# Kernel optimization log

Hardware: AMD Instinct MI355X
Metric: run time of the kernel (lower is better)

The kernel has to match this reference:

```python
import jax, jax.numpy as jnp
import numpy as np

N = 65536   # batch_size * timeseries
D = 512     # feature dim of h_real
K = 64      # n_clusters


def setup_inputs() -> dict:
    key = jax.random.key(0)
    k1, k2 = jax.random.split(key)
    h_real = jax.random.normal(k1, (N, D), dtype=jnp.float32)
    # F is an (approximately) orthogonal projection parameter [N, K].
    F = jax.random.normal(k2, (N, K), dtype=jnp.float32)
    return {"h_real": h_real, "F": F}


def reference(h_real, F):
    # Original: WTW = h h^T (N x N); loss = trace(WTW) - trace(F^T WTW F).
    # Algebraically identical reduced form, never materializing the N x N Gram:
    #   trace(h h^T) = sum(h * h)
    #   trace(F^T h h^T F) = ||F^T h||_F^2
    tr_wtw = jnp.sum(h_real * h_real)
    G = F.T @ h_real                      # [K, D] skinny GEMM
    tr_proj = jnp.sum(G * G)
    return tr_wtw - tr_proj
```

## Files before the change

kernel.cpp:

```cpp
#include <hip/hip_runtime.h>
#include <hip/hip_fp16.h>

#define N_TOT 65536
#define D_DIM 512
#define K_DIM 64
#define NC    32
#define HT_S  40
#define GSZ   (K_DIM * D_DIM)

typedef __bf16   bf16x8 __attribute__((ext_vector_type(8)));
typedef float    f32x4  __attribute__((ext_vector_type(4)));
typedef _Float16 half8  __attribute__((ext_vector_type(8)));

__device__ __forceinline__ unsigned int pack_bf16(float a, float b) {
    union { float f; unsigned int u; } x, y;
    x.f = a; y.f = b;
    unsigned int lo = (x.u + 0x7fffu + ((x.u >> 16) & 1u)) >> 16;
    unsigned int hi = (y.u + 0x7fffu + ((y.u >> 16) & 1u)) >> 16;
    return lo | (hi << 16);
}

extern "C" __global__ void __launch_bounds__(1024)
k1_partial(const float* __restrict__ h, const float* __restrict__ F,
           float* __restrict__ trw_out, unsigned short* __restrict__ gpart,
           float* __restrict__ out, int rowsPerBlock) {
    __shared__ unsigned short ht[2][D_DIM * HT_S];
    __shared__ unsigned short Ft[2][K_DIM * HT_S];
    __shared__ float red[16];

    const int tid = threadIdx.x;
    const int b   = blockIdx.x;
    if (b == 0 && tid == 0) out[0] = 0.0f;

    const int row0    = b * rowsPerBlock;
    const int nChunks = rowsPerBlock / NC;

    const int sd = tid & 511;
    const int sg = tid >> 9;
    const int fk = tid & 63;
    const int fg = (tid >> 6) & 3;
    const int wave = tid >> 6;
    const int lane = tid & 63;
    const int m    = lane & 15;
    const int q    = lane >> 4;

    f32x4 acc[4][2];
    #pragma unroll
    for (int kt = 0; kt < 4; ++kt)
        #pragma unroll
        for (int dt = 0; dt < 2; ++dt)
            acc[kt][dt] = (f32x4){0.f, 0.f, 0.f, 0.f};

    float trw = 0.f;

    auto stage = [&](int c, int p) {
        const int r0 = row0 + c * NC;
        const float* hb = h + (size_t)r0 * D_DIM + sd;
        #pragma unroll
        for (int gi = 0; gi < 2; ++gi) {
            const int g8 = gi * 2 + sg;
            float v[8];
            #pragma unroll
            for (int j = 0; j < 8; ++j) {
                v[j] = hb[(size_t)(g8 * 8 + j) * D_DIM];
                trw += v[j] * v[j];
            }
            uint4 pk;
            pk.x = pack_bf16(v[0], v[1]);
            pk.y = pack_bf16(v[2], v[3]);
            pk.z = pack_bf16(v[4], v[5]);
            pk.w = pack_bf16(v[6], v[7]);
            *(uint4*)&ht[p][sd * HT_S + g8 * 8] = pk;
        }
        if (tid < 256) {
            const float* fb = F + (size_t)r0 * K_DIM + fk;
            float w[8];
            #pragma unroll
            for (int j = 0; j < 8; ++j)
                w[j] = fb[(size_t)(fg * 8 + j) * K_DIM];
            uint4 pk;
            pk.x = pack_bf16(w[0], w[1]);
            pk.y = pack_bf16(w[2], w[3]);
            pk.z = pack_bf16(w[4], w[5]);
            pk.w = pack_bf16(w[6], w[7]);
            *(uint4*)&Ft[p][fk * HT_S + fg * 8] = pk;
        }
    };

    stage(0, 0);

    for (int c = 0; c < nChunks; ++c) {
        __syncthreads();
        if (c + 1 < nChunks) stage(c + 1, (c + 1) & 1);

        const int p = c & 1;
        bf16x8 bfrag[2], afrag[4];
        #pragma unroll
        for (int dt = 0; dt < 2; ++dt)
            bfrag[dt] = *(const bf16x8*)&ht[p][(wave * 32 + dt * 16 + m) * HT_S + q * 8];
        #pragma unroll
        for (int kt = 0; kt < 4; ++kt)
            afrag[kt] = *(const bf16x8*)&Ft[p][(kt * 16 + m) * HT_S + q * 8];
        #pragma unroll
        for (int kt = 0; kt < 4; ++kt)
            #pragma unroll
            for (int dt = 0; dt < 2; ++dt)
                acc[kt][dt] = __builtin_amdgcn_mfma_f32_16x16x32_bf16(
                    afrag[kt], bfrag[dt], acc[kt][dt], 0, 0, 0);
    }

    unsigned short* gp = gpart + (size_t)b * GSZ;
    #pragma unroll
    for (int kt = 0; kt < 4; ++kt)
        #pragma unroll
        for (int dt = 0; dt < 2; ++dt)
            #pragma unroll
            for (int r = 0; r < 4; ++r) {
                const int k = kt * 16 + q * 4 + r;
                const int d = wave * 32 + dt * 16 + m;
                __half hv = __float2half(acc[kt][dt][r]);
                gp[k * D_DIM + d] = *(unsigned short*)&hv;
            }

    #pragma unroll
    for (int off = 32; off > 0; off >>= 1) trw += __shfl_down(trw, off, 64);
    if (lane == 0) red[wave] = trw;
    __syncthreads();
    if (tid == 0) {
        float s = 0.f;
        #pragma unroll
        for (int w = 0; w < 16; ++w) s += red[w];
        trw_out[b] = s;
    }
}

extern "C" __global__ void __launch_bounds__(512)
k2_reduce(const float* __restrict__ trw, const unsigned short* __restrict__ gpart,
          float* __restrict__ out, int P) {
    __shared__ float sh[32 * 16 * 8];
    __shared__ float red2[8];

    const int tid = threadIdx.x;
    const int sub = tid >> 4;
    const int oct = tid & 15;
    const int tt  = blockIdx.x * 16 + oct;

    float g[8];
    #pragma unroll
    for (int j = 0; j < 8; ++j) g[j] = 0.f;

    const unsigned short* base = gpart + (size_t)tt * 8;
    for (int b = sub; b < P; b += 32) {
        half8 v = *(const half8*)(base + (size_t)b * GSZ);
        #pragma unroll
        for (int j = 0; j < 8; ++j) g[j] += (float)v[j];
    }
    #pragma unroll
    for (int j = 0; j < 8; ++j) sh[(sub * 16 + oct) * 8 + j] = g[j];
    __syncthreads();

    float val = 0.f;
    if (tid < 128) {
        const int o2 = tid >> 3, j = tid & 7;
        float s = 0.f;
        #pragma unroll
        for (int sb = 0; sb < 32; ++sb) s += sh[(sb * 16 + o2) * 8 + j];
        val = -s * s;
    } else if (blockIdx.x == 0 && tid - 128 < P) {
        val = trw[tid - 128];
    }

    #pragma unroll
    for (int off = 32; off > 0; off >>= 1) val += __shfl_down(val, off, 64);
    if ((tid & 63) == 0) red2[tid >> 6] = val;
    __syncthreads();
    if (tid == 0) {
        float s = 0.f;
        #pragma unroll
        for (int w = 0; w < 8; ++w) s += red2[w];
        atomicAdd(out, s);
    }
}

extern "C" void kernel_launch(void* const* d_in, const int* in_sizes, int n_in,
                              void* d_out, int out_size, void* d_ws, size_t ws_size,
                              hipStream_t stream) {
    const float* h = (const float*)d_in[0];
    const float* F = (const float*)d_in[1];
    float* out = (float*)d_out;

    int P = 256;
    while (P > 1 && (size_t)4096 + (size_t)P * (GSZ * 2) > ws_size) P >>= 1;
    const int rowsPerBlock = N_TOT / P;

    float* trw = (float*)d_ws;
    unsigned short* gpart = (unsigned short*)((char*)d_ws + 4096);

    hipLaunchKernelGGL(k1_partial, dim3(P), dim3(1024), 0, stream,
                       h, F, trw, gpart, out, rowsPerBlock);
    hipLaunchKernelGGL(k2_reduce, dim3(256), dim3(512), 0, stream,
                       trw, gpart, out, P);
}
```

Measured before the change: 210.9 us.

## Load MFMA fragments directly from global memory, dropping LDS staging

```diff
diff --git a/kernel.cpp b/kernel.cpp
--- a/kernel.cpp
+++ b/kernel.cpp
@@ -5,7 +5,6 @@
 #define D_DIM 512
 #define K_DIM 64
 #define NC    32
-#define HT_S  40
 #define GSZ   (K_DIM * D_DIM)
 
 typedef __bf16   bf16x8 __attribute__((ext_vector_type(8)));
@@ -20,29 +19,25 @@
     return lo | (hi << 16);
 }
 
+union pk4 { unsigned int u[4]; bf16x8 v; };
+
 extern "C" __global__ void __launch_bounds__(1024)
 k1_partial(const float* __restrict__ h, const float* __restrict__ F,
            float* __restrict__ trw_out, unsigned short* __restrict__ gpart,
            float* __restrict__ out, int rowsPerBlock) {
-    __shared__ unsigned short ht[2][D_DIM * HT_S];
-    __shared__ unsigned short Ft[2][K_DIM * HT_S];
     __shared__ float red[16];
 
     const int tid = threadIdx.x;
     const int b   = blockIdx.x;
     if (b == 0 && tid == 0) out[0] = 0.0f;
 
-    const int row0    = b * rowsPerBlock;
-    const int nChunks = rowsPerBlock / NC;
-
-    const int sd = tid & 511;
-    const int sg = tid >> 9;
-    const int fk = tid & 63;
-    const int fg = (tid >> 6) & 3;
     const int wave = tid >> 6;
     const int lane = tid & 63;
     const int m    = lane & 15;
     const int q    = lane >> 4;
+
+    const int row0    = b * rowsPerBlock;
+    const int nChunks = rowsPerBlock / NC;
 
     f32x4 acc[4][2];
     #pragma unroll
@@ -53,60 +48,58 @@
 
     float trw = 0.f;
 
-    auto stage = [&](int c, int p) {
-        const int r0 = row0 + c * NC;
-        const float* hb = h + (size_t)r0 * D_DIM + sd;
+    const float* hb = h + (size_t)(row0 + q * 8) * D_DIM + wave * 32 + m;
+    const float* fb = F + (size_t)(row0 + q * 8) * K_DIM + m;
+
+    for (int c = 0; c < nChunks; ++c) {
+        float vb[16];
         #pragma unroll
-        for (int gi = 0; gi < 2; ++gi) {
-            const int g8 = gi * 2 + sg;
-            float v[8];
-            #pragma unroll
-            for (int j = 0; j < 8; ++j) {
-                v[j] = hb[(size_t)(g8 * 8 + j) * D_DIM];
-                trw += v[j] * v[j];
-            }
-            uint4 pk;
-            pk.x = pack_bf16(v[0], v[1]);
-            pk.y = pack_bf16(v[2], v[3]);
-            pk.z = pack_bf16(v[4], v[5]);
-            pk.w = pack_bf16(v[6], v[7]);
-            *(uint4*)&ht[p][sd * HT_S + g8 * 8] = pk;
-        }
-        if (tid < 256) {
-            const float* fb = F + (size_t)r0 * K_DIM + fk;
-            float w[8];
+        for (int dt = 0; dt < 2; ++dt)
             #pragma unroll
             for (int j = 0; j < 8; ++j)
-                w[j] = fb[(size_t)(fg * 8 + j) * K_DIM];
-            uint4 pk;
-            pk.x = pack_bf16(w[0], w[1]);
-            pk.y = pack_bf16(w[2], w[3]);
-            pk.z = pack_bf16(w[4], w[5]);
-            pk.w = pack_bf16(w[6], w[7]);
-            *(uint4*)&Ft[p][fk * HT_S + fg * 8] = pk;
+                vb[dt * 8 + j] = hb[(size_t)j * D_DIM + dt * 16];
+
+        bf16x8 bfrag[2];
+        #pragma unroll
+        for (int dt = 0; dt < 2; ++dt) {
+            pk4 p;
+            #pragma unroll
+            for (int jj = 0; jj < 4; ++jj) {
+                float a0 = vb[dt * 8 + 2 * jj], a1 = vb[dt * 8 + 2 * jj + 1];
+                trw += a0 * a0 + a1 * a1;
+                p.u[jj] = pack_bf16(a0, a1);
+            }
+            bfrag[dt] = p.v;
         }
-    };
 
-    stage(0, 0);
+        bf16x8 afrag[4];
+        #pragma unroll
+        for (int r = 0; r < 2; ++r) {
+            float va[16];
+            #pragma unroll
+            for (int kk = 0; kk < 2; ++kk)
+                #pragma unroll
+                for (int j = 0; j < 8; ++j)
+                    va[kk * 8 + j] = fb[(size_t)j * K_DIM + (r * 2 + kk) * 16];
+            #pragma unroll
+            for (int kk = 0; kk < 2; ++kk) {
+                pk4 p;
+                #pragma unroll
+                for (int jj = 0; jj < 4; ++jj)
+                    p.u[jj] = pack_bf16(va[kk * 8 + 2 * jj], va[kk * 8 + 2 * jj + 1]);
+                afrag[r * 2 + kk] = p.v;
+            }
+        }
 
-    for (int c = 0; c < nChunks; ++c) {
-        __syncthreads();
-        if (c + 1 < nChunks) stage(c + 1, (c + 1) & 1);
-
-        const int p = c & 1;
-        bf16x8 bfrag[2], afrag[4];
-        #pragma unroll
-        for (int dt = 0; dt < 2; ++dt)
-            bfrag[dt] = *(const bf16x8*)&ht[p][(wave * 32 + dt * 16 + m) * HT_S + q * 8];
-        #pragma unroll
-        for (int kt = 0; kt < 4; ++kt)
-            afrag[kt] = *(const bf16x8*)&Ft[p][(kt * 16 + m) * HT_S + q * 8];
         #pragma unroll
         for (int kt = 0; kt < 4; ++kt)
             #pragma unroll
             for (int dt = 0; dt < 2; ++dt)
                 acc[kt][dt] = __builtin_amdgcn_mfma_f32_16x16x32_bf16(
                     afrag[kt], bfrag[dt], acc[kt][dt], 0, 0, 0);
+
+        hb += (size_t)NC * D_DIM;
+        fb += (size_t)NC * K_DIM;
     }
 
     unsigned short* gp = gpart + (size_t)b * GSZ;
```

After: 216.7 us. +2.8%, slower.
